# Kernel optimization log

Hardware: AMD Instinct MI355X
Metric: run time of the kernel (lower is better)

The kernel has to match this reference:

```python
import jax, jax.numpy as jnp
import numpy as np

D_MODEL = 2048
N_HEADS = 16
N_KV_HEADS = 4
HEAD_DIM = D_MODEL // N_HEADS
KV_DIM = N_KV_HEADS * HEAD_DIM
EPS = 1e-6


def setup_inputs() -> dict:
    key = jax.random.key(0)
    ks = jax.random.split(key, 5)
    N, L = 4, 2048
    x = jax.random.normal(ks[0], (N, L, D_MODEL), dtype=jnp.float32)
    Wqkv = jax.random.normal(ks[1], (D_MODEL, D_MODEL + 2 * KV_DIM), dtype=jnp.float32) * (1.0 / np.sqrt(D_MODEL))
    bqkv = jnp.zeros((D_MODEL + 2 * KV_DIM,), dtype=jnp.float32)
    Wout = jax.random.normal(ks[2], (D_MODEL, D_MODEL), dtype=jnp.float32) * (1.0 / np.sqrt(D_MODEL))
    bout = jnp.zeros((D_MODEL,), dtype=jnp.float32)
    q_scale = jnp.ones((HEAD_DIM,), dtype=jnp.float32)
    k_scale = jnp.ones((HEAD_DIM,), dtype=jnp.float32)
    return {"x": x, "Wqkv": Wqkv, "bqkv": bqkv, "q_scale": q_scale, "k_scale": k_scale, "Wout": Wout, "bout": bout}


def _rmsnorm(x, scale):
    return x * (scale / jnp.sqrt(jnp.mean(jnp.square(x), axis=-1, keepdims=True) + EPS))


def reference(x, Wqkv, bqkv, q_scale, k_scale, Wout, bout):
    N, L, D = x.shape
    qkv = x @ Wqkv + bqkv  # [N, L, D + 2*kv_dim]
    q = qkv[..., :D].reshape(N, L, N_HEADS, HEAD_DIM).transpose(0, 2, 1, 3)          # [N,H,L,hd]
    k = qkv[..., D:D + KV_DIM].reshape(N, L, N_KV_HEADS, HEAD_DIM).transpose(0, 2, 1, 3)  # [N,Hkv,L,hd]
    v = qkv[..., D + KV_DIM:].reshape(N, L, N_KV_HEADS, HEAD_DIM).transpose(0, 2, 1, 3)
    q = _rmsnorm(q, q_scale)
    k = _rmsnorm(k, k_scale)
    # GQA expand (repeat_interleave over head dim)
    n_rep = N_HEADS // N_KV_HEADS
    k = jnp.repeat(k, n_rep, axis=1)
    v = jnp.repeat(v, n_rep, axis=1)
    scale = 1.0 / jnp.sqrt(jnp.float32(HEAD_DIM))
    scores = jnp.einsum("nhqd,nhkd->nhqk", q, k) * scale  # [N,H,L,L]
    causal = jnp.tril(jnp.ones((L, L), dtype=bool))
    scores = jnp.where(causal, scores, jnp.finfo(scores.dtype).min)
    attn = jax.nn.softmax(scores, axis=-1)
    y = jnp.einsum("nhqk,nhkd->nhqd", attn, v)  # [N,H,L,hd]
    y = y.transpose(0, 2, 1, 3).reshape(N, L, D)
    return y @ Wout + bout
```

## Files before the change

kernel.cpp:

```cpp
#include <hip/hip_runtime.h>

typedef unsigned int uint_t;
typedef unsigned short ushort_t;

using f32x4 = __attribute__((ext_vector_type(4))) float;
using bf16x8 = __attribute__((ext_vector_type(8))) short;

#define D_MODEL 2048
#define N_HEADS 16
#define N_KV    4
#define HD      128
#define KV_DIM  (N_KV * HD)
#define NQKV    (D_MODEL + 2*KV_DIM)
#define SEQ     2048
#define NB      4
#define MROWS   (NB * SEQ)
#define SM_SCALE 0.08838834764831845f

__device__ __forceinline__ ushort_t f2bf(float f) {
    uint_t u = __float_as_uint(f);
    u = (u + 0x7FFFu + ((u >> 16) & 1u)) >> 16;
    return (ushort_t)u;
}

__device__ __forceinline__ void gload16(const ushort_t* g, ushort_t* l) {
    __builtin_amdgcn_global_load_lds(
        (const __attribute__((address_space(1))) unsigned int*)g,
        (__attribute__((address_space(3))) unsigned int*)l, 16, 0, 0);
}

__global__ __launch_bounds__(256) void conv_x_kernel(const float* __restrict__ in,
                                                     ushort_t* __restrict__ out, int n) {
    int i = (blockIdx.x * 256 + threadIdx.x) * 4;
    if (i >= n) return;
    float4 v = *(const float4*)&in[i];
    ushort_t o[4] = {f2bf(v.x), f2bf(v.y), f2bf(v.z), f2bf(v.w)};
    *(uint2*)&out[i] = *(uint2*)o;
}

__global__ __launch_bounds__(256) void conv_wt_kernel(const float* __restrict__ W,
                                                      ushort_t* __restrict__ WT,
                                                      int K, int Nout) {
    __shared__ float tile[32][33];
    int n0 = blockIdx.x * 32, k0 = blockIdx.y * 32;
    int tx = threadIdx.x, ty = threadIdx.y;
    for (int i = 0; i < 4; ++i)
        tile[ty + 8*i][tx] = W[(size_t)(k0 + ty + 8*i) * Nout + n0 + tx];
    __syncthreads();
    for (int i = 0; i < 4; ++i)
        WT[(size_t)(n0 + ty + 8*i) * K + k0 + tx] = f2bf(tile[tx][ty + 8*i]);
}

__global__ __launch_bounds__(256) void vt_kernel(const ushort_t* __restrict__ Vn,
                                                 ushort_t* __restrict__ Vt) {
    __shared__ ushort_t tile[64][72];
    int l0 = blockIdx.x * 64, d0 = blockIdx.y * 64;
    int nk = blockIdx.z;
    int t = threadIdx.x;
    for (int i = 0; i < 2; ++i) {
        int idx = t + i * 256;
        int rr = idx >> 3, c = idx & 7;
        uint4 v = *(const uint4*)&Vn[((size_t)nk * SEQ + l0 + rr) * HD + d0 + c * 8];
        *(uint4*)&tile[rr][c * 8] = v;
    }
    __syncthreads();
    for (int i = 0; i < 2; ++i) {
        int idx = t + i * 256;
        int dr = idx >> 3, c2 = idx & 7;
        ushort_t o[8];
        for (int j = 0; j < 8; ++j) o[j] = tile[c2 * 8 + j][dr];
        *(uint4*)&Vt[((size_t)nk * HD + d0 + dr) * SEQ + l0 + c2 * 8] = *(uint4*)o;
    }
}

#define GEMM_MAIN_LOOP(A, BT, K)                                                   \
    for (int k0 = 0; k0 < K; k0 += 64) {                                           \
        for (int i = 0; i < 4; ++i) {                                              \
            int ci = (w * 4 + i) * 64 + lane;                                      \
            int row = ci >> 3, c = ci & 7, cg = c ^ (row & 7);                     \
            gload16(&A [(size_t)(bm + row) * K + k0 + cg * 8], &As[0][0] + (w * 4 + i) * 512); \
            gload16(&BT[(size_t)(bn + row) * K + k0 + cg * 8], &Bs[0][0] + (w * 4 + i) * 512); \
        }                                                                          \
        __syncthreads();                                                           \
        for (int kk = 0; kk < 64; kk += 32) {                                      \
            bf16x8 af[4], bfr[4];                                                  \
            int k4 = kk >> 3;                                                      \
            for (int i = 0; i < 4; ++i)                                            \
                af[i]  = *(const bf16x8*)&As[mb + i * 16 + r][((k4 + quad) ^ (r & 7)) * 8]; \
            for (int j = 0; j < 4; ++j)                                            \
                bfr[j] = *(const bf16x8*)&Bs[nb + j * 16 + r][((k4 + quad) ^ (r & 7)) * 8]; \
            for (int i = 0; i < 4; ++i)                                            \
                for (int j = 0; j < 4; ++j)                                        \
                    acc[i][j] = __builtin_amdgcn_mfma_f32_16x16x32_bf16(af[i], bfr[j], acc[i][j], 0, 0, 0); \
        }                                                                          \
        __syncthreads();                                                           \
    }

__global__ __launch_bounds__(256) void gemm_bt_kernel(const ushort_t* __restrict__ A,
                                                      const ushort_t* __restrict__ BT,
                                                      const float* __restrict__ bias,
                                                      float* __restrict__ C,
                                                      int M, int N, int K) {
    __shared__ ushort_t As[128][64];
    __shared__ ushort_t Bs[128][64];
    const int bm = blockIdx.x * 128, bn = blockIdx.y * 128;
    const int t = threadIdx.x;
    const int w = t >> 6, lane = t & 63, quad = lane >> 4, r = lane & 15;
    const int mb = (w >> 1) * 64, nb = (w & 1) * 64;
    f32x4 acc[4][4] = {};
    GEMM_MAIN_LOOP(A, BT, K)
    for (int i = 0; i < 4; ++i)
        for (int j = 0; j < 4; ++j)
            for (int reg = 0; reg < 4; ++reg) {
                int row = bm + mb + i * 16 + quad * 4 + reg;
                int col = bn + nb + j * 16 + r;
                C[(size_t)row * N + col] = acc[i][j][reg] + bias[col];
            }
}

__global__ __launch_bounds__(256) void gemm_qkv_kernel(const ushort_t* __restrict__ A,
                                                       const ushort_t* __restrict__ BT,
                                                       const float* __restrict__ bias,
                                                       const float* __restrict__ q_scale,
                                                       const float* __restrict__ k_scale,
                                                       ushort_t* __restrict__ Q,
                                                       ushort_t* __restrict__ Kb,
                                                       ushort_t* __restrict__ Vn) {
    __shared__ ushort_t As[128][64];
    __shared__ ushort_t Bs[128][64];
    __shared__ float ssum[2][128];
    const int K = D_MODEL;
    const int bm = blockIdx.x * 128, bn = blockIdx.y * 128;
    const int t = threadIdx.x;
    const int w = t >> 6, lane = t & 63, quad = lane >> 4, r = lane & 15;
    const int mb = (w >> 1) * 64, nb = (w & 1) * 64;
    f32x4 acc[4][4] = {};
    GEMM_MAIN_LOOP(A, BT, K)

    const int g = blockIdx.y;
    float bj[4];
    for (int j = 0; j < 4; ++j) bj[j] = bias[bn + nb + j * 16 + r];
    for (int i = 0; i < 4; ++i)
        for (int j = 0; j < 4; ++j)
            for (int reg = 0; reg < 4; ++reg) acc[i][j][reg] += bj[j];

    const int n = bm >> 11, lb = bm & 2047;
    if (g < 20) {
        for (int i = 0; i < 4; ++i)
            for (int reg = 0; reg < 4; ++reg) {
                float p = 0.f;
                for (int j = 0; j < 4; ++j) p += acc[i][j][reg] * acc[i][j][reg];
                p += __shfl_xor(p, 1); p += __shfl_xor(p, 2);
                p += __shfl_xor(p, 4); p += __shfl_xor(p, 8);
                if (r == 0) ssum[w & 1][mb + i * 16 + quad * 4 + reg] = p;
            }
        __syncthreads();
        const float* scp = (g < 16) ? q_scale : k_scale;
        const float smul = (g < 16) ? SM_SCALE : 1.0f;
        float scj[4];
        for (int j = 0; j < 4; ++j) scj[j] = scp[nb + j * 16 + r];
        ushort_t* dst = (g < 16) ? (Q  + (size_t)(n * 16 + g) * SEQ * HD)
                                 : (Kb + (size_t)(n * 4 + g - 16) * SEQ * HD);
        for (int i = 0; i < 4; ++i)
            for (int reg = 0; reg < 4; ++reg) {
                int rl = mb + i * 16 + quad * 4 + reg;
                float ss = ssum[0][rl] + ssum[1][rl];
                float iv = rsqrtf(ss * (1.0f / 128.0f) + 1e-6f) * smul;
                size_t lrow = lb + rl;
                for (int j = 0; j < 4; ++j) {
                    int d = nb + j * 16 + r;
                    dst[lrow * HD + d] = f2bf(acc[i][j][reg] * iv * scj[j]);
                }
            }
    } else {
        ushort_t* dst = Vn + (size_t)(n * 4 + g - 20) * SEQ * HD;
        for (int i = 0; i < 4; ++i)
            for (int reg = 0; reg < 4; ++reg) {
                size_t lrow = lb + mb + i * 16 + quad * 4 + reg;
                for (int j = 0; j < 4; ++j) {
                    int d = nb + j * 16 + r;
                    dst[lrow * HD + d] = f2bf(acc[i][j][reg]);
                }
            }
    }
}

__global__ __launch_bounds__(256, 2) void attn_kernel(const ushort_t* __restrict__ Q,
                                                      const ushort_t* __restrict__ K,
                                                      const ushort_t* __restrict__ Vt,
                                                      ushort_t* __restrict__ Y) {
    const int pid = blockIdx.x, h = blockIdx.y, n = blockIdx.z;
    const int kvh = h >> 2;
    const ushort_t* Qp = Q  + (size_t)(n * N_HEADS + h) * SEQ * HD;
    const ushort_t* Kp = K  + (size_t)(n * N_KV + kvh) * SEQ * HD;
    const ushort_t* Vp = Vt + (size_t)(n * N_KV + kvh) * HD * SEQ;

    __shared__ ushort_t Ks[64][128];
    __shared__ ushort_t Vts[128][64];
    __shared__ ushort_t Ps[128][64];

    const int t = threadIdx.x, w = t >> 6, lane = t & 63, quad = lane >> 4, r = lane & 15;

    for (int rep = 0; rep < 2; ++rep) {
        const int qt = rep ? (15 - pid) : pid;
        const int q0 = qt * 128;

        bf16x8 aq[2][4];
        for (int s = 0; s < 2; ++s)
            for (int kc = 0; kc < 4; ++kc)
                aq[s][kc] = *(const bf16x8*)&Qp[(size_t)(q0 + w * 32 + s * 16 + r) * HD + kc * 32 + quad * 8];

        f32x4 oacc[2][8] = {};
        float lsum[2][4] = {};
        const int nct = 2 * qt + 2;

        for (int ct = 0; ct < nct; ++ct) {
            __syncthreads();
            for (int i = 0; i < 4; ++i) {
                int ci = (w * 4 + i) * 64 + lane;
                {
                    int row = ci >> 4, c = ci & 15, cg = c ^ (row & 7);
                    gload16(&Kp[(size_t)(ct * 64 + row) * HD + cg * 8], &Ks[0][0] + (w * 4 + i) * 512);
                }
                {
                    int row = ci >> 3, c = ci & 7, cg = c ^ (row & 7);
                    gload16(&Vp[(size_t)row * SEQ + ct * 64 + cg * 8], &Vts[0][0] + (w * 4 + i) * 512);
                }
            }
            __syncthreads();

            f32x4 sacc[2][4] = {};
            for (int kc = 0; kc < 4; ++kc)
                for (int jt = 0; jt < 4; ++jt) {
                    bf16x8 bk = *(const bf16x8*)&Ks[jt * 16 + r][((kc * 4 + quad) ^ (r & 7)) * 8];
                    sacc[0][jt] = __builtin_amdgcn_mfma_f32_16x16x32_bf16(aq[0][kc], bk, sacc[0][jt], 0, 0, 0);
                    sacc[1][jt] = __builtin_amdgcn_mfma_f32_16x16x32_bf16(aq[1][kc], bk, sacc[1][jt], 0, 0, 0);
                }

            const bool diag = (ct >= 2 * qt);
            for (int s = 0; s < 2; ++s)
                for (int reg = 0; reg < 4; ++reg) {
                    int prow = w * 32 + s * 16 + quad * 4 + reg;
                    int qg = q0 + prow;
                    float rs = 0.f;
                    for (int jt = 0; jt < 4; ++jt) {
                        float sv = sacc[s][jt][reg];
                        if (diag && (ct * 64 + jt * 16 + r) > qg) sv = -1e30f;
                        float p = __expf(sv);
                        rs += p;
                        Ps[prow][(jt * 16 + r) ^ (quad << 4)] = (ushort_t)(__float_as_uint(p) >> 16);
                    }
                    lsum[s][reg] += rs;
                }

            for (int kk = 0; kk < 64; kk += 32) {
                bf16x8 pa[2];
                for (int s = 0; s < 2; ++s)
                    pa[s] = *(const bf16x8*)&Ps[w * 32 + s * 16 + r][(kk + quad * 8) ^ (((r >> 2) & 3) << 4)];
                for (int dt = 0; dt < 8; ++dt) {
                    bf16x8 bv = *(const bf16x8*)&Vts[dt * 16 + r][(((kk >> 3) + quad) ^ (r & 7)) * 8];
                    oacc[0][dt] = __builtin_amdgcn_mfma_f32_16x16x32_bf16(pa[0], bv, oacc[0][dt], 0, 0, 0);
                    oacc[1][dt] = __builtin_amdgcn_mfma_f32_16x16x32_bf16(pa[1], bv, oacc[1][dt], 0, 0, 0);
                }
            }
        }

        for (int s = 0; s < 2; ++s)
            for (int reg = 0; reg < 4; ++reg) {
                float sv = lsum[s][reg];
                for (int m = 1; m < 16; m <<= 1) sv += __shfl_xor(sv, m);
                float invl = 1.0f / sv;
                int lrow = q0 + w * 32 + s * 16 + quad * 4 + reg;
                size_t base = ((size_t)(n * SEQ + lrow)) * D_MODEL + h * HD;
                for (int dt = 0; dt < 8; ++dt)
                    Y[base + dt * 16 + r] = f2bf(oacc[s][dt][reg] * invl);
            }
    }
}

extern "C" void kernel_launch(void* const* d_in, const int* in_sizes, int n_in,
                              void* d_out, int out_size, void* d_ws, size_t ws_size,
                              hipStream_t stream) {
    const float* x       = (const float*)d_in[0];
    const float* Wqkv    = (const float*)d_in[1];
    const float* bqkv    = (const float*)d_in[2];
    const float* q_scale = (const float*)d_in[3];
    const float* k_scale = (const float*)d_in[4];
    const float* Wout    = (const float*)d_in[5];
    const float* bout    = (const float*)d_in[6];
    float* out = (float*)d_out;

    ushort_t* xb  = (ushort_t*)d_ws;
    ushort_t* WT  = xb  + (size_t)MROWS * D_MODEL;
    ushort_t* Qb  = WT  + (size_t)NQKV * D_MODEL;
    ushort_t* Kb  = Qb  + (size_t)NB * N_HEADS * SEQ * HD;
    ushort_t* Vnb = Kb  + (size_t)NB * N_KV * SEQ * HD;
    ushort_t* Vtb = Vnb + (size_t)NB * N_KV * SEQ * HD;

    conv_x_kernel<<<MROWS * D_MODEL / 1024, 256, 0, stream>>>(x, xb, MROWS * D_MODEL);
    conv_wt_kernel<<<dim3(NQKV / 32, D_MODEL / 32), dim3(32, 8), 0, stream>>>(Wqkv, WT, D_MODEL, NQKV);
    gemm_qkv_kernel<<<dim3(MROWS / 128, NQKV / 128), 256, 0, stream>>>(xb, WT, bqkv, q_scale, k_scale, Qb, Kb, Vnb);
    vt_kernel<<<dim3(SEQ / 64, HD / 64, NB * N_KV), 256, 0, stream>>>(Vnb, Vtb);
    conv_wt_kernel<<<dim3(D_MODEL / 32, D_MODEL / 32), dim3(32, 8), 0, stream>>>(Wout, WT, D_MODEL, D_MODEL);
    attn_kernel<<<dim3(8, N_HEADS, NB), 256, 0, stream>>>(Qb, Kb, Vtb, xb);
    gemm_bt_kernel<<<dim3(MROWS / 128, D_MODEL / 128), 256, 0, stream>>>(xb, WT, bout, out, MROWS, D_MODEL, D_MODEL);
}
```

Measured before the change: 474.9 us.

## Double-buffer GEMM and attention K tiles, fuse V transpose into QKV epilogue

The GEMM main loop now double-buffers the A and B tiles in LDS, prefetching the next K-slice while MFMAs run on the current one, and the RMSnorm reduction reuses the A buffer as scratch. The QKV GEMM epilogue writes V directly in transposed layout, which removes the separate vt_kernel and its intermediate buffer. The attention kernel moves to 128 threads with 64 query rows per wave, double-buffers K tiles, and lets each wave skip causally masked tiles. The costs are double the GEMM LDS footprint, higher register pressure in attention, and strided V stores.

```diff
diff --git a/kernel.cpp b/kernel.cpp
--- a/kernel.cpp
+++ b/kernel.cpp
@@ -51,49 +51,34 @@
         WT[(size_t)(n0 + ty + 8*i) * K + k0 + tx] = f2bf(tile[tx][ty + 8*i]);
 }
 
-__global__ __launch_bounds__(256) void vt_kernel(const ushort_t* __restrict__ Vn,
-                                                 ushort_t* __restrict__ Vt) {
-    __shared__ ushort_t tile[64][72];
-    int l0 = blockIdx.x * 64, d0 = blockIdx.y * 64;
-    int nk = blockIdx.z;
-    int t = threadIdx.x;
-    for (int i = 0; i < 2; ++i) {
-        int idx = t + i * 256;
-        int rr = idx >> 3, c = idx & 7;
-        uint4 v = *(const uint4*)&Vn[((size_t)nk * SEQ + l0 + rr) * HD + d0 + c * 8];
-        *(uint4*)&tile[rr][c * 8] = v;
+#define GEMM_STAGE(A, BT, k0, b)                                                   \
+    for (int i = 0; i < 4; ++i) {                                                  \
+        int ci = (w * 4 + i) * 64 + lane;                                          \
+        int row = ci >> 3, c = ci & 7, cg = c ^ (row & 7);                         \
+        gload16(&A [(size_t)(bm + row) * K + (k0) + cg * 8], &As[b][0][0] + (w * 4 + i) * 512); \
+        gload16(&BT[(size_t)(bn + row) * K + (k0) + cg * 8], &Bs[b][0][0] + (w * 4 + i) * 512); \
     }
-    __syncthreads();
-    for (int i = 0; i < 2; ++i) {
-        int idx = t + i * 256;
-        int dr = idx >> 3, c2 = idx & 7;
-        ushort_t o[8];
-        for (int j = 0; j < 8; ++j) o[j] = tile[c2 * 8 + j][dr];
-        *(uint4*)&Vt[((size_t)nk * HD + d0 + dr) * SEQ + l0 + c2 * 8] = *(uint4*)o;
-    }
-}
 
 #define GEMM_MAIN_LOOP(A, BT, K)                                                   \
-    for (int k0 = 0; k0 < K; k0 += 64) {                                           \
-        for (int i = 0; i < 4; ++i) {                                              \
-            int ci = (w * 4 + i) * 64 + lane;                                      \
-            int row = ci >> 3, c = ci & 7, cg = c ^ (row & 7);                     \
-            gload16(&A [(size_t)(bm + row) * K + k0 + cg * 8], &As[0][0] + (w * 4 + i) * 512); \
-            gload16(&BT[(size_t)(bn + row) * K + k0 + cg * 8], &Bs[0][0] + (w * 4 + i) * 512); \
+    GEMM_STAGE(A, BT, 0, 0)                                                        \
+    {                                                                              \
+        int buf = 0;                                                               \
+        for (int k0 = 0; k0 < K; k0 += 64) {                                       \
+            __syncthreads();                     \
+            if (k0 + 64 < K) { GEMM_STAGE(A, BT, k0 + 64, buf ^ 1) }               \
+            for (int kk = 0; kk < 64; kk += 32) {                                  \
+                bf16x8 af[4], bfr[4];                                              \
+                int k4 = kk >> 3;                                                  \
+                for (int i = 0; i < 4; ++i)                                        \
+                    af[i]  = *(const bf16x8*)&As[buf][mb + i * 16 + r][((k4 + quad) ^ (r & 7)) * 8]; \
+                for (int j = 0; j < 4; ++j)                                        \
+                    bfr[j] = *(const bf16x8*)&Bs[buf][nb + j * 16 + r][((k4 + quad) ^ (r & 7)) * 8]; \
+                for (int i = 0; i < 4; ++i)                                        \
+                    for (int j = 0; j < 4; ++j)                                    \
+                        acc[i][j] = __builtin_amdgcn_mfma_f32_16x16x32_bf16(af[i], bfr[j], acc[i][j], 0, 0, 0); \
+            }                                                                      \
+            buf ^= 1;                                                              \
         }                                                                          \
-        __syncthreads();                                                           \
-        for (int kk = 0; kk < 64; kk += 32) {                                      \
-            bf16x8 af[4], bfr[4];                                                  \
-            int k4 = kk >> 3;                                                      \
-            for (int i = 0; i < 4; ++i)                                            \
-                af[i]  = *(const bf16x8*)&As[mb + i * 16 + r][((k4 + quad) ^ (r & 7)) * 8]; \
-            for (int j = 0; j < 4; ++j)                                            \
-                bfr[j] = *(const bf16x8*)&Bs[nb + j * 16 + r][((k4 + quad) ^ (r & 7)) * 8]; \
-            for (int i = 0; i < 4; ++i)                                            \
-                for (int j = 0; j < 4; ++j)                                        \
-                    acc[i][j] = __builtin_amdgcn_mfma_f32_16x16x32_bf16(af[i], bfr[j], acc[i][j], 0, 0, 0); \
-        }                                                                          \
-        __syncthreads();                                                           \
     }
 
 __global__ __launch_bounds__(256) void gemm_bt_kernel(const ushort_t* __restrict__ A,
@@ -101,8 +86,8 @@
                                                       const float* __restrict__ bias,
                                                       float* __restrict__ C,
                                                       int M, int N, int K) {
-    __shared__ ushort_t As[128][64];
-    __shared__ ushort_t Bs[128][64];
+    __shared__ ushort_t As[2][128][64];
+    __shared__ ushort_t Bs[2][128][64];
     const int bm = blockIdx.x * 128, bn = blockIdx.y * 128;
     const int t = threadIdx.x;
     const int w = t >> 6, lane = t & 63, quad = lane >> 4, r = lane & 15;
@@ -125,10 +110,9 @@
                                                        const float* __restrict__ k_scale,
                                                        ushort_t* __restrict__ Q,
                                                        ushort_t* __restrict__ Kb,
-                                                       ushort_t* __restrict__ Vn) {
-    __shared__ ushort_t As[128][64];
-    __shared__ ushort_t Bs[128][64];
-    __shared__ float ssum[2][128];
+                                                       ushort_t* __restrict__ Vt) {
+    __shared__ ushort_t As[2][128][64];
+    __shared__ ushort_t Bs[2][128][64];
     const int K = D_MODEL;
     const int bm = blockIdx.x * 128, bn = blockIdx.y * 128;
     const int t = threadIdx.x;
@@ -146,13 +130,15 @@
 
     const int n = bm >> 11, lb = bm & 2047;
     if (g < 20) {
+        __syncthreads();
+        float* ssum = (float*)&As[0][0][0];
         for (int i = 0; i < 4; ++i)
             for (int reg = 0; reg < 4; ++reg) {
                 float p = 0.f;
                 for (int j = 0; j < 4; ++j) p += acc[i][j][reg] * acc[i][j][reg];
                 p += __shfl_xor(p, 1); p += __shfl_xor(p, 2);
                 p += __shfl_xor(p, 4); p += __shfl_xor(p, 8);
-                if (r == 0) ssum[w & 1][mb + i * 16 + quad * 4 + reg] = p;
+                if (r == 0) ssum[(w & 1) * 128 + mb + i * 16 + quad * 4 + reg] = p;
             }
         __syncthreads();
         const float* scp = (g < 16) ? q_scale : k_scale;
@@ -164,7 +150,7 @@
         for (int i = 0; i < 4; ++i)
             for (int reg = 0; reg < 4; ++reg) {
                 int rl = mb + i * 16 + quad * 4 + reg;
-                float ss = ssum[0][rl] + ssum[1][rl];
+                float ss = ssum[rl] + ssum[128 + rl];
                 float iv = rsqrtf(ss * (1.0f / 128.0f) + 1e-6f) * smul;
                 size_t lrow = lb + rl;
                 for (int j = 0; j < 4; ++j) {
@@ -173,19 +159,18 @@
                 }
             }
     } else {
-        ushort_t* dst = Vn + (size_t)(n * 4 + g - 20) * SEQ * HD;
+        ushort_t* dstT = Vt + (size_t)(n * 4 + g - 20) * HD * SEQ;
         for (int i = 0; i < 4; ++i)
-            for (int reg = 0; reg < 4; ++reg) {
-                size_t lrow = lb + mb + i * 16 + quad * 4 + reg;
-                for (int j = 0; j < 4; ++j) {
-                    int d = nb + j * 16 + r;
-                    dst[lrow * HD + d] = f2bf(acc[i][j][reg]);
-                }
+            for (int j = 0; j < 4; ++j) {
+                int d = nb + j * 16 + r;
+                ushort_t o[4];
+                for (int reg = 0; reg < 4; ++reg) o[reg] = f2bf(acc[i][j][reg]);
+                *(uint2*)&dstT[(size_t)d * SEQ + lb + mb + i * 16 + quad * 4] = *(uint2*)o;
             }
     }
 }
 
-__global__ __launch_bounds__(256, 2) void attn_kernel(const ushort_t* __restrict__ Q,
+__global__ __launch_bounds__(128, 1) void attn_kernel(const ushort_t* __restrict__ Q,
                                                       const ushort_t* __restrict__ K,
                                                       const ushort_t* __restrict__ Vt,
                                                       ushort_t* __restrict__ Y) {
@@ -195,82 +180,99 @@
     const ushort_t* Kp = K  + (size_t)(n * N_KV + kvh) * SEQ * HD;
     const ushort_t* Vp = Vt + (size_t)(n * N_KV + kvh) * HD * SEQ;
 
-    __shared__ ushort_t Ks[64][128];
+    __shared__ ushort_t Ks[2][64][128];
     __shared__ ushort_t Vts[128][64];
     __shared__ ushort_t Ps[128][64];
 
-    const int t = threadIdx.x, w = t >> 6, lane = t & 63, quad = lane >> 4, r = lane & 15;
+    const int t = threadIdx.x, w2 = t >> 6, lane = t & 63, quad = lane >> 4, r = lane & 15;
 
     for (int rep = 0; rep < 2; ++rep) {
         const int qt = rep ? (15 - pid) : pid;
         const int q0 = qt * 128;
 
-        bf16x8 aq[2][4];
-        for (int s = 0; s < 2; ++s)
+        __syncthreads();
+        for (int i = 0; i < 8; ++i) {
+            int ci = (w2 * 8 + i) * 64 + lane;
+            int row = ci >> 4, c = ci & 15, cg = c ^ (row & 7);
+            gload16(&Kp[(size_t)row * HD + cg * 8], &Ks[0][0][0] + (w2 * 8 + i) * 512);
+        }
+
+        bf16x8 aq[4][4];
+        for (int s = 0; s < 4; ++s)
             for (int kc = 0; kc < 4; ++kc)
-                aq[s][kc] = *(const bf16x8*)&Qp[(size_t)(q0 + w * 32 + s * 16 + r) * HD + kc * 32 + quad * 8];
-
-        f32x4 oacc[2][8] = {};
-        float lsum[2][4] = {};
+                aq[s][kc] = *(const bf16x8*)&Qp[(size_t)(q0 + w2 * 64 + s * 16 + r) * HD + kc * 32 + quad * 8];
+
+        f32x4 oacc[4][8] = {};
+        float lsum[4][4] = {};
         const int nct = 2 * qt + 2;
+        int buf = 0;
 
         for (int ct = 0; ct < nct; ++ct) {
             __syncthreads();
-            for (int i = 0; i < 4; ++i) {
-                int ci = (w * 4 + i) * 64 + lane;
-                {
+            for (int i = 0; i < 8; ++i) {
+                int ci = (w2 * 8 + i) * 64 + lane;
+                int row = ci >> 3, c = ci & 7, cg = c ^ (row & 7);
+                gload16(&Vp[(size_t)row * SEQ + ct * 64 + cg * 8], &Vts[0][0] + (w2 * 8 + i) * 512);
+            }
+            if (ct + 1 < nct) {
+                for (int i = 0; i < 8; ++i) {
+                    int ci = (w2 * 8 + i) * 64 + lane;
                     int row = ci >> 4, c = ci & 15, cg = c ^ (row & 7);
-                    gload16(&Kp[(size_t)(ct * 64 + row) * HD + cg * 8], &Ks[0][0] + (w * 4 + i) * 512);
+                    gload16(&Kp[(size_t)((ct + 1) * 64 + row) * HD + cg * 8],
+                            &Ks[buf ^ 1][0][0] + (w2 * 8 + i) * 512);
                 }
-                {
-                    int row = ci >> 3, c = ci & 7, cg = c ^ (row & 7);
-                    gload16(&Vp[(size_t)row * SEQ + ct * 64 + cg * 8], &Vts[0][0] + (w * 4 + i) * 512);
+            }
+
+            const bool active = (ct <= 2 * qt + w2);
+            if (active) {
+                f32x4 sacc[4][4] = {};
+                for (int kc = 0; kc < 4; ++kc)
+                    for (int jt = 0; jt < 4; ++jt) {
+                        bf16x8 bk = *(const bf16x8*)&Ks[buf][jt * 16 + r][((kc * 4 + quad) ^ (r & 7)) * 8];
+                        for (int s = 0; s < 4; ++s)
+                            sacc[s][jt] = __builtin_amdgcn_mfma_f32_16x16x32_bf16(aq[s][kc], bk, sacc[s][jt], 0, 0, 0);
+                    }
+                const bool diag = (ct == 2 * qt + w2);
+                for (int s = 0; s < 4; ++s)
+                    for (int reg = 0; reg < 4; ++reg) {
+                        int prow = w2 * 64 + s * 16 + quad * 4 + reg;
+                        int qg = q0 + prow;
+                        float rs = 0.f;
+                        for (int jt = 0; jt < 4; ++jt) {
+                            float sv = sacc[s][jt][reg];
+                            if (diag && (ct * 64 + jt * 16 + r) > qg) sv = -1e30f;
+                            float p = __expf(sv);
+                            rs += p;
+                            int colp = ((((jt * 2 + (r >> 3)) ^ prow) & 7) << 3) | (r & 7);
+                            Ps[prow][colp] = (ushort_t)(__float_as_uint(p) >> 16);
+                        }
+                        lsum[s][reg] += rs;
+                    }
+            }
+            __syncthreads();
+            if (active) {
+                for (int kk = 0; kk < 64; kk += 32) {
+                    bf16x8 pa[4];
+                    for (int s = 0; s < 4; ++s) {
+                        int row = w2 * 64 + s * 16 + r;
+                        pa[s] = *(const bf16x8*)&Ps[row][((((kk >> 3) + quad) ^ row) & 7) * 8];
+                    }
+                    for (int dt = 0; dt < 8; ++dt) {
+                        bf16x8 bv = *(const bf16x8*)&Vts[dt * 16 + r][((((kk >> 3) + quad) ^ (r & 7)) & 7) * 8];
+                        for (int s = 0; s < 4; ++s)
+                            oacc[s][dt] = __builtin_amdgcn_mfma_f32_16x16x32_bf16(pa[s], bv, oacc[s][dt], 0, 0, 0);
+                    }
                 }
             }
-            __syncthreads();
-
-            f32x4 sacc[2][4] = {};
-            for (int kc = 0; kc < 4; ++kc)
-                for (int jt = 0; jt < 4; ++jt) {
-                    bf16x8 bk = *(const bf16x8*)&Ks[jt * 16 + r][((kc * 4 + quad) ^ (r & 7)) * 8];
-                    sacc[0][jt] = __builtin_amdgcn_mfma_f32_16x16x32_bf16(aq[0][kc], bk, sacc[0][jt], 0, 0, 0);
-                    sacc[1][jt] = __builtin_amdgcn_mfma_f32_16x16x32_bf16(aq[1][kc], bk, sacc[1][jt], 0, 0, 0);
-                }
-
-            const bool diag = (ct >= 2 * qt);
-            for (int s = 0; s < 2; ++s)
-                for (int reg = 0; reg < 4; ++reg) {
-                    int prow = w * 32 + s * 16 + quad * 4 + reg;
-                    int qg = q0 + prow;
-                    float rs = 0.f;
-                    for (int jt = 0; jt < 4; ++jt) {
-                        float sv = sacc[s][jt][reg];
-                        if (diag && (ct * 64 + jt * 16 + r) > qg) sv = -1e30f;
-                        float p = __expf(sv);
-                        rs += p;
-                        Ps[prow][(jt * 16 + r) ^ (quad << 4)] = (ushort_t)(__float_as_uint(p) >> 16);
-                    }
-                    lsum[s][reg] += rs;
-                }
-
-            for (int kk = 0; kk < 64; kk += 32) {
-                bf16x8 pa[2];
-                for (int s = 0; s < 2; ++s)
-                    pa[s] = *(const bf16x8*)&Ps[w * 32 + s * 16 + r][(kk + quad * 8) ^ (((r >> 2) & 3) << 4)];
-                for (int dt = 0; dt < 8; ++dt) {
-                    bf16x8 bv = *(const bf16x8*)&Vts[dt * 16 + r][(((kk >> 3) + quad) ^ (r & 7)) * 8];
-                    oacc[0][dt] = __builtin_amdgcn_mfma_f32_16x16x32_bf16(pa[0], bv, oacc[0][dt], 0, 0, 0);
-                    oacc[1][dt] = __builtin_amdgcn_mfma_f32_16x16x32_bf16(pa[1], bv, oacc[1][dt], 0, 0, 0);
-                }
-            }
+            buf ^= 1;
         }
 
-        for (int s = 0; s < 2; ++s)
+        for (int s = 0; s < 4; ++s)
             for (int reg = 0; reg < 4; ++reg) {
                 float sv = lsum[s][reg];
                 for (int m = 1; m < 16; m <<= 1) sv += __shfl_xor(sv, m);
                 float invl = 1.0f / sv;
-                int lrow = q0 + w * 32 + s * 16 + quad * 4 + reg;
+                int lrow = q0 + w2 * 64 + s * 16 + quad * 4 + reg;
                 size_t base = ((size_t)(n * SEQ + lrow)) * D_MODEL + h * HD;
                 for (int dt = 0; dt < 8; ++dt)
                     Y[base + dt * 16 + r] = f2bf(oacc[s][dt][reg] * invl);
@@ -294,14 +296,12 @@
     ushort_t* WT  = xb  + (size_t)MROWS * D_MODEL;
     ushort_t* Qb  = WT  + (size_t)NQKV * D_MODEL;
     ushort_t* Kb  = Qb  + (size_t)NB * N_HEADS * SEQ * HD;
-    ushort_t* Vnb = Kb  + (size_t)NB * N_KV * SEQ * HD;
-    ushort_t* Vtb = Vnb + (size_t)NB * N_KV * SEQ * HD;
+    ushort_t* Vtb = Kb  + (size_t)NB * N_KV * SEQ * HD;
 
     conv_x_kernel<<<MROWS * D_MODEL / 1024, 256, 0, stream>>>(x, xb, MROWS * D_MODEL);
     conv_wt_kernel<<<dim3(NQKV / 32, D_MODEL / 32), dim3(32, 8), 0, stream>>>(Wqkv, WT, D_MODEL, NQKV);
-    gemm_qkv_kernel<<<dim3(MROWS / 128, NQKV / 128), 256, 0, stream>>>(xb, WT, bqkv, q_scale, k_scale, Qb, Kb, Vnb);
-    vt_kernel<<<dim3(SEQ / 64, HD / 64, NB * N_KV), 256, 0, stream>>>(Vnb, Vtb);
+    gemm_qkv_kernel<<<dim3(MROWS / 128, NQKV / 128), 256, 0, stream>>>(xb, WT, bqkv, q_scale, k_scale, Qb, Kb, Vtb);
     conv_wt_kernel<<<dim3(D_MODEL / 32, D_MODEL / 32), dim3(32, 8), 0, stream>>>(Wout, WT, D_MODEL, D_MODEL);
-    attn_kernel<<<dim3(8, N_HEADS, NB), 256, 0, stream>>>(Qb, Kb, Vtb, xb);
+    attn_kernel<<<dim3(8, N_HEADS, NB), 128, 0, stream>>>(Qb, Kb, Vtb, xb);
     gemm_bt_kernel<<<dim3(MROWS / 128, D_MODEL / 128), 256, 0, stream>>>(xb, WT, bout, out, MROWS, D_MODEL, D_MODEL);
 }
```

Result: slower. 643.6 us (+35.5%).
